# Kernel tuning notes

Hardware: AMD Instinct MI355X
Metric: run time of the kernel (lower is better)

Reference implementation:

```python
import jax, jax.numpy as jnp
import numpy as np
from jax import lax

ORDER = 2  # diffusion order per support, as in __init__(order=2)


def setup_inputs() -> dict:
    key = jax.random.key(0)
    k1, k2, k3 = jax.random.split(key, 3)
    N, C, V, L = 64, 32, 512, 13
    S, Kt, C_out = 3, 3, 32
    C_cat = (ORDER * S + 1) * C  # 224
    x = jax.random.normal(k1, (N, C, V, L), dtype=jnp.float32)
    support = jax.random.uniform(k2, (S, V, V), dtype=jnp.float32)
    # Conv2d(c_in=224, c_out=32, kernel=(1,Kt)) weights, PyTorch OIHW layout
    W = jax.random.normal(k3, (C_out, C_cat, 1, Kt), dtype=jnp.float32) * 0.02
    b = jnp.zeros((C_out,), dtype=jnp.float32)
    return {"x": x, "support": support, "W": W, "b": b}


def _nconv(x, A):
    # torch: A = A.T; einsum('ncvl,vw->ncwl', x, A.T)
    # => out[n,c,w,l] = sum_v A[w,v] * x[n,c,v,l]
    return jnp.einsum('ncvl,wv->ncwl', x, A)


def reference(x, support, W, b):
    out = [x]
    for s in range(support.shape[0]):  # small fixed support_len=3
        A = support[s]
        x1 = _nconv(x, A)
        out.append(x1)
        for _ in range(2, ORDER + 1):
            x1 = _nconv(x1, A)
            out.append(x1)
    h = jnp.concatenate(out, axis=1)  # [N, (order*S+1)*C, V, L]
    # Conv2d kernel (1, Kt), no padding, stride 1 -> temporal conv
    y = lax.conv_general_dilated(
        h, W, window_strides=(1, 1), padding='VALID',
        dimension_numbers=('NCHW', 'OIHW', 'NCHW'))
    y = y + b[None, :, None, None]
    # dropout is identity in eval mode
    return y
```

## Files before the change

kernel.cpp:

```cpp
#include <hip/hip_runtime.h>

typedef __attribute__((ext_vector_type(4))) float f32x4;
typedef __attribute__((ext_vector_type(8))) __bf16 bf16x8;
typedef __attribute__((ext_vector_type(4))) __bf16 bf16x4;
typedef __attribute__((ext_vector_type(4))) int i32x4;

#define SXE (26624 * 512)

__global__ __launch_bounds__(256)
void prep_x(const float* __restrict__ x, __bf16* __restrict__ Xv2,
            const float* __restrict__ A, __bf16* __restrict__ Ab) {
  const int vt = blockIdx.x, n = blockIdx.y, tid = threadIdx.x;
  if (vt < 12) {
    const int i = (n * 12 + vt) * 256 + tid;
    const float4 f = ((const float4*)A)[i];
    bf16x4 o;
    o[0] = (__bf16)f.x; o[1] = (__bf16)f.y; o[2] = (__bf16)f.z; o[3] = (__bf16)f.w;
    ((bf16x4*)Ab)[i] = o;
  }
  __shared__ float Xs[32 * 209];
  const float* src = x + ((size_t)n * 32) * 6656 + vt * 16 * 13;
  for (int i = tid; i < 32 * 208; i += 256) {
    const int c = i / 208, r = i - c * 208;
    Xs[c * 209 + r] = src[(size_t)c * 6656 + r];
  }
  __syncthreads();
  for (int j = tid; j < 416; j += 256) {
    const int c = j & 31, l = j >> 5;
    bf16x8 o8[2];
    #pragma unroll
    for (int v = 0; v < 16; ++v) o8[v >> 3][v & 7] = (__bf16)Xs[c * 209 + v * 13 + l];
    __bf16* d = Xv2 + (((size_t)n * 13 + l) * 32 + c) * 512 + vt * 16;
    *(bf16x8*)d = o8[0];
    *(bf16x8*)(d + 8) = o8[1];
  }
}

__global__ __launch_bounds__(512, 2)
void gemm_bf16(const __bf16* __restrict__ Ab, const __bf16* __restrict__ SRC,
               __bf16* __restrict__ DSTB, size_t srcStride, size_t dstStride, int cpx) {
  extern __shared__ char gsm[];
  const int tid = threadIdx.x;
  const int lane = tid & 63, wid = tid >> 6, q = lane >> 4, r16 = lane & 15;

  const int bid = blockIdx.x;
  const int lg = (bid & 7) * cpx + (bid >> 3);
  const int bx = lg / 6, r6 = lg % 6, s = r6 >> 1, by = r6 & 1;

  const __bf16* Amat = Ab + (size_t)s * 512 * 512;
  const __bf16* B = SRC + (size_t)s * srcStride;
  __bf16* D = DSTB + (size_t)s * dstStride;

  const int W0 = by * 256, B0 = bx * 256;
  const int wm = wid >> 2, wn = wid & 3;
  const int srow = lane >> 3, spos = lane & 7;

  f32x4 acc[8][4];
  #pragma unroll
  for (int m = 0; m < 8; ++m)
    #pragma unroll
    for (int n = 0; n < 4; ++n) acc[m][n] = {0.f, 0.f, 0.f, 0.f};

  auto STAGE = [&](int bufsel, int kt) {
    const int k0 = kt * 64;
    char* As = gsm + bufsel * 65536;
    char* Bs = As + 32768;
    #pragma unroll
    for (int i = 0; i < 4; ++i) {
      const int slot = i * 8 + wid;
      const int r = slot * 8 + srow;
      const int gc = spos ^ (r & 7);
      const __bf16* ga = Amat + (size_t)(W0 + r) * 512 + k0 + gc * 8;
      const __bf16* gb = B    + (size_t)(B0 + r) * 512 + k0 + gc * 8;
      __builtin_amdgcn_global_load_lds((const __attribute__((address_space(1))) unsigned int*)ga,
                                       (__attribute__((address_space(3))) unsigned int*)(As + slot * 1024 + lane * 16),
                                       16, 0, 0);
      __builtin_amdgcn_global_load_lds((const __attribute__((address_space(1))) unsigned int*)gb,
                                       (__attribute__((address_space(3))) unsigned int*)(Bs + slot * 1024 + lane * 16),
                                       16, 0, 0);
    }
  };

  STAGE(0, 0);
  __syncthreads();

  for (int t = 0; t < 8; ++t) {
    const int cur = t & 1;
    if (t < 7) STAGE(cur ^ 1, t + 1);
    const char* As = gsm + cur * 65536;
    const char* Bs = As + 32768;
    #pragma unroll
    for (int ks = 0; ks < 2; ++ks) {
      const int ch = ks * 4 + q;
      bf16x8 af[4], df[8];
      #pragma unroll
      for (int n = 0; n < 4; ++n) {
        const int r = wn * 64 + n * 16 + r16;
        af[n] = *(const bf16x8*)(As + r * 128 + ((ch ^ (r & 7)) << 4));
      }
      #pragma unroll
      for (int m = 0; m < 8; ++m) {
        const int r = wm * 128 + m * 16 + r16;
        df[m] = *(const bf16x8*)(Bs + r * 128 + ((ch ^ (r & 7)) << 4));
      }
      __builtin_amdgcn_s_setprio(1);
      #pragma unroll
      for (int m = 0; m < 8; ++m)
        #pragma unroll
        for (int n = 0; n < 4; ++n)
          acc[m][n] = __builtin_amdgcn_mfma_f32_16x16x32_bf16(af[n], df[m], acc[m][n], 0, 0, 0);
      __builtin_amdgcn_s_setprio(0);
    }
    __syncthreads();
  }

  #pragma unroll
  for (int m = 0; m < 8; ++m) {
    const int b = B0 + wm * 128 + m * 16 + r16;
    #pragma unroll
    for (int n = 0; n < 4; ++n) {
      const int w = W0 + wn * 64 + n * 16 + q * 4;
      bf16x4 o4;
      o4[0] = (__bf16)acc[m][n][0]; o4[1] = (__bf16)acc[m][n][1];
      o4[2] = (__bf16)acc[m][n][2]; o4[3] = (__bf16)acc[m][n][3];
      *(bf16x4*)(D + (size_t)b * 512 + w) = o4;
    }
  }
}

__global__ __launch_bounds__(256, 2)
void conv_kernel(const __bf16* __restrict__ Xv2, const __bf16* __restrict__ Y1,
                 const __bf16* __restrict__ Y2, const float* __restrict__ W,
                 const float* __restrict__ bias, float* __restrict__ y) {
  const int vt = blockIdx.x;
  const int n  = blockIdx.y;
  const int tid = threadIdx.x;
  const int lane = tid & 63, wave = tid >> 6, q = lane >> 4, r16 = lane & 15;

  __shared__ char sm[59392];
  char* Ws = sm + 53248;

  const __bf16* gsrc[7] = {Xv2, Y1, Y2, Y1 + (size_t)SXE, Y2 + (size_t)SXE,
                           Y1 + 2 * (size_t)SXE, Y2 + 2 * (size_t)SXE};

  f32x4 acc[11][2];
  #pragma unroll
  for (int t = 0; t < 11; ++t) { acc[t][0] = {0,0,0,0}; acc[t][1] = {0,0,0,0}; }

  const int vv = wave * 16 + r16;
  const int vch = vv >> 3;
  const int vlo = (vv & 7) * 2;
  const int cst = tid >> 3, hst = tid & 7;
  const size_t goff = ((size_t)cst << 9) + hst * 8;
  const int lds_off = cst * 128 + ((hst ^ ((cst >> 3) << 1)) << 4);
  const int gbase = q * 1024 + (((vch ^ (q << 1)) & 7) << 4) + vlo;

  const size_t base = ((size_t)n * 416) * 512 + vt * 64;

  i32x4 hreg[13];
  {
    const __bf16* src = gsrc[0] + base;
    #pragma unroll
    for (int l = 0; l < 13; ++l)
      hreg[l] = *(const i32x4*)(src + (size_t)l * 16384 + goff);
  }

  for (int g = 0; g < 7; ++g) {
    __syncthreads();
    #pragma unroll
    for (int l = 0; l < 13; ++l)
      *(i32x4*)(sm + l * 4096 + lds_off) = hreg[l];
    for (int idx = tid; idx < 768; idx += 256) {
      const int f = idx >> 7, rem2 = idx & 127, lw = rem2 >> 1, half = rem2 & 1;
      const int kt = f >> 1, of = f & 1;
      const int o = of * 16 + (lw & 15);
      const int cc = g * 32 + (lw >> 4) * 8 + half * 4;
      bf16x4 w4;
      #pragma unroll
      for (int j = 0; j < 4; ++j)
        w4[j] = (__bf16)W[((size_t)o * 224 + cc + j) * 3 + kt];
      *(bf16x4*)(Ws + idx * 8) = w4;
    }
    __syncthreads();

    if (g < 6) {
      const __bf16* srcn = gsrc[g + 1] + base;
      #pragma unroll
      for (int l = 0; l < 13; ++l)
        hreg[l] = *(const i32x4*)(srcn + (size_t)l * 16384 + goff);
    }

    bf16x8 a8[13];
    #pragma unroll
    for (int l = 0; l < 13; ++l) {
      bf16x8 a;
      #pragma unroll
      for (int j = 0; j < 8; ++j)
        a[j] = *(const __bf16*)(sm + l * 4096 + gbase + j * 128);
      a8[l] = a;
    }
    bf16x8 wf[6];
    #pragma unroll
    for (int f = 0; f < 6; ++f)
      wf[f] = *(const bf16x8*)(Ws + (f * 64 + lane) * 16);

    #pragma unroll
    for (int kt = 0; kt < 3; ++kt)
      #pragma unroll
      for (int of = 0; of < 2; ++of)
        #pragma unroll
        for (int t = 0; t < 11; ++t)
          acc[t][of] = __builtin_amdgcn_mfma_f32_16x16x32_bf16(a8[t + kt], wf[kt * 2 + of], acc[t][of], 0, 0, 0);
  }

  float* Ds = (float*)sm;
  const int o16 = lane & 15;
  #pragma unroll
  for (int p = 0; p < 2; ++p) {
    __syncthreads();
    #pragma unroll
    for (int t = 0; t < 11; ++t) {
      const int vbase = wave * 16 + q * 4;
      #pragma unroll
      for (int rg = 0; rg < 4; ++rg)
        Ds[o16 * 708 + (vbase + rg) * 11 + t] = acc[t][p][rg];
    }
    __syncthreads();
    #pragma unroll
    for (int i = 0; i < 11; ++i) {
      const int cg = tid + i * 256;
      const int oo = cg / 176, ch = cg - oo * 176;
      f32x4 v4 = *(const f32x4*)(Ds + oo * 708 + ch * 4);
      const float bo = bias[p * 16 + oo];
      v4[0] += bo; v4[1] += bo; v4[2] += bo; v4[3] += bo;
      float* yp = y + (((size_t)n * 32 + p * 16 + oo) * 512 + vt * 64) * 11 + ch * 4;
      *(f32x4*)yp = v4;
    }
  }
}

extern "C" void kernel_launch(void* const* d_in, const int* in_sizes, int n_in,
                              void* d_out, int out_size, void* d_ws, size_t ws_size,
                              hipStream_t stream) {
  (void)in_sizes; (void)n_in; (void)out_size; (void)ws_size;
  const float* x = (const float*)d_in[0];
  const float* A = (const float*)d_in[1];
  const float* W = (const float*)d_in[2];
  const float* b = (const float*)d_in[3];
  float* y = (float*)d_out;

  char* ws = (char*)d_ws;
  const size_t SXB = (size_t)SXE * 2;
  __bf16* Xv2 = (__bf16*)ws;
  __bf16* Y1  = (__bf16*)(ws + SXB);
  __bf16* Y2  = (__bf16*)(ws + 4 * SXB);
  __bf16* Ab  = (__bf16*)(ws + 7 * SXB);

  prep_x<<<dim3(32, 64), 256, 0, stream>>>(x, Xv2, A, Ab);
  gemm_bf16<<<dim3(624), 512, 131072, stream>>>(Ab, Xv2, Y1, 0, (size_t)SXE, 78);
  gemm_bf16<<<dim3(624), 512, 131072, stream>>>(Ab, Y1, Y2, (size_t)SXE, (size_t)SXE, 78);
  conv_kernel<<<dim3(8, 64), 256, 0, stream>>>(Xv2, Y1, Y2, W, b, y);
}
```

Measured before the change: 208.6 us.

## Precompute squared supports and compute both diffusion hops in one GEMM launch

Adds a transpose kernel and a small GEMM that form A² for each support in bf16. The two dependent diffusion GEMM launches become a single launch that multiplies X by both A and A², writing all six outputs. The aim is to remove the serial dependency between the hops and reduce launch and tail overhead. In exchange it adds two small launches, one of which uses only 12 blocks, and rounds A² to bf16, which changes numerics slightly. The transposed and squared matrices are kept temporarily in the output buffer.

Result: no change. 208.8 us (+0.1%).

```diff
diff --git a/kernel.cpp b/kernel.cpp
--- a/kernel.cpp
+++ b/kernel.cpp
@@ -6,6 +6,7 @@
 typedef __attribute__((ext_vector_type(4))) int i32x4;
 
 #define SXE (26624 * 512)
+#define AMS 262144
 
 __global__ __launch_bounds__(256)
 void prep_x(const float* __restrict__ x, __bf16* __restrict__ Xv2,
@@ -36,20 +37,35 @@
   }
 }
 
+__global__ __launch_bounds__(256)
+void transA(const float* __restrict__ A, __bf16* __restrict__ Abt) {
+  const int ut = blockIdx.x, vt = blockIdx.y, s = blockIdx.z, tid = threadIdx.x;
+  __shared__ float T[64][65];
+  const float* Asrc = A + (size_t)s * AMS;
+  #pragma unroll
+  for (int p = 0; p < 16; ++p) {
+    const int rv = p * 4 + (tid >> 6), cu = tid & 63;
+    T[rv][cu] = Asrc[(size_t)(vt * 64 + rv) * 512 + ut * 64 + cu];
+  }
+  __syncthreads();
+  #pragma unroll
+  for (int p = 0; p < 16; ++p) {
+    const int ru = p * 4 + (tid >> 6), cv = tid & 63;
+    Abt[(size_t)s * AMS + (size_t)(ut * 64 + ru) * 512 + vt * 64 + cv] = (__bf16)T[cv][ru];
+  }
+}
+
 __global__ __launch_bounds__(512, 2)
-void gemm_bf16(const __bf16* __restrict__ Ab, const __bf16* __restrict__ SRC,
-               __bf16* __restrict__ DSTB, size_t srcStride, size_t dstStride, int cpx) {
+void gemm_asq(const __bf16* __restrict__ Abt, const __bf16* __restrict__ Ab,
+              __bf16* __restrict__ Ab2) {
   extern __shared__ char gsm[];
   const int tid = threadIdx.x;
   const int lane = tid & 63, wid = tid >> 6, q = lane >> 4, r16 = lane & 15;
-
-  const int bid = blockIdx.x;
-  const int lg = (bid & 7) * cpx + (bid >> 3);
-  const int bx = lg / 6, r6 = lg % 6, s = r6 >> 1, by = r6 & 1;
-
-  const __bf16* Amat = Ab + (size_t)s * 512 * 512;
-  const __bf16* B = SRC + (size_t)s * srcStride;
-  __bf16* D = DSTB + (size_t)s * dstStride;
+  const int bx = blockIdx.x, by = blockIdx.y, s = blockIdx.z;
+
+  const __bf16* Amat = Abt + (size_t)s * AMS;
+  const __bf16* B = Ab + (size_t)s * AMS;
+  __bf16* D = Ab2 + (size_t)s * AMS;
 
   const int W0 = by * 256, B0 = bx * 256;
   const int wm = wid >> 2, wn = wid & 3;
@@ -83,6 +99,94 @@
 
   STAGE(0, 0);
   __syncthreads();
+  for (int t = 0; t < 8; ++t) {
+    const int cur = t & 1;
+    if (t < 7) STAGE(cur ^ 1, t + 1);
+    const char* As = gsm + cur * 65536;
+    const char* Bs = As + 32768;
+    #pragma unroll
+    for (int ks = 0; ks < 2; ++ks) {
+      const int ch = ks * 4 + q;
+      bf16x8 af[4], df[8];
+      #pragma unroll
+      for (int n = 0; n < 4; ++n) {
+        const int r = wn * 64 + n * 16 + r16;
+        af[n] = *(const bf16x8*)(As + r * 128 + ((ch ^ (r & 7)) << 4));
+      }
+      #pragma unroll
+      for (int m = 0; m < 8; ++m) {
+        const int r = wm * 128 + m * 16 + r16;
+        df[m] = *(const bf16x8*)(Bs + r * 128 + ((ch ^ (r & 7)) << 4));
+      }
+      #pragma unroll
+      for (int m = 0; m < 8; ++m)
+        #pragma unroll
+        for (int n = 0; n < 4; ++n)
+          acc[m][n] = __builtin_amdgcn_mfma_f32_16x16x32_bf16(af[n], df[m], acc[m][n], 0, 0, 0);
+    }
+    __syncthreads();
+  }
+  #pragma unroll
+  for (int m = 0; m < 8; ++m) {
+    const int b = B0 + wm * 128 + m * 16 + r16;
+    #pragma unroll
+    for (int n = 0; n < 4; ++n) {
+      const int w = W0 + wn * 64 + n * 16 + q * 4;
+      bf16x4 o4;
+      o4[0] = (__bf16)acc[m][n][0]; o4[1] = (__bf16)acc[m][n][1];
+      o4[2] = (__bf16)acc[m][n][2]; o4[3] = (__bf16)acc[m][n][3];
+      *(bf16x4*)(D + (size_t)b * 512 + w) = o4;
+    }
+  }
+}
+
+__global__ __launch_bounds__(512, 2)
+void gemm_bf16(const __bf16* __restrict__ Ab, const __bf16* __restrict__ Ab2,
+               const __bf16* __restrict__ SRC, __bf16* __restrict__ Yb, int cpx) {
+  extern __shared__ char gsm[];
+  const int tid = threadIdx.x;
+  const int lane = tid & 63, wid = tid >> 6, q = lane >> 4, r16 = lane & 15;
+
+  const int bid = blockIdx.x;
+  const int lg = (bid & 7) * cpx + (bid >> 3);
+  const int bx = lg / 12, r12 = lg % 12, z = r12 >> 1, by = r12 & 1;
+
+  const __bf16* Amat = (z < 3) ? (Ab + (size_t)z * AMS) : (Ab2 + (size_t)(z - 3) * AMS);
+  const __bf16* B = SRC;
+  __bf16* D = Yb + (size_t)z * SXE;
+
+  const int W0 = by * 256, B0 = bx * 256;
+  const int wm = wid >> 2, wn = wid & 3;
+  const int srow = lane >> 3, spos = lane & 7;
+
+  f32x4 acc[8][4];
+  #pragma unroll
+  for (int m = 0; m < 8; ++m)
+    #pragma unroll
+    for (int n = 0; n < 4; ++n) acc[m][n] = {0.f, 0.f, 0.f, 0.f};
+
+  auto STAGE = [&](int bufsel, int kt) {
+    const int k0 = kt * 64;
+    char* As = gsm + bufsel * 65536;
+    char* Bs = As + 32768;
+    #pragma unroll
+    for (int i = 0; i < 4; ++i) {
+      const int slot = i * 8 + wid;
+      const int r = slot * 8 + srow;
+      const int gc = spos ^ (r & 7);
+      const __bf16* ga = Amat + (size_t)(W0 + r) * 512 + k0 + gc * 8;
+      const __bf16* gb = B    + (size_t)(B0 + r) * 512 + k0 + gc * 8;
+      __builtin_amdgcn_global_load_lds((const __attribute__((address_space(1))) unsigned int*)ga,
+                                       (__attribute__((address_space(3))) unsigned int*)(As + slot * 1024 + lane * 16),
+                                       16, 0, 0);
+      __builtin_amdgcn_global_load_lds((const __attribute__((address_space(1))) unsigned int*)gb,
+                                       (__attribute__((address_space(3))) unsigned int*)(Bs + slot * 1024 + lane * 16),
+                                       16, 0, 0);
+    }
+  };
+
+  STAGE(0, 0);
+  __syncthreads();
 
   for (int t = 0; t < 8; ++t) {
     const int cur = t & 1;
@@ -255,9 +359,12 @@
   __bf16* Y1  = (__bf16*)(ws + SXB);
   __bf16* Y2  = (__bf16*)(ws + 4 * SXB);
   __bf16* Ab  = (__bf16*)(ws + 7 * SXB);
+  __bf16* Ab2 = (__bf16*)d_out;
+  __bf16* Abt = (__bf16*)((char*)d_out + (4 << 20));
 
   prep_x<<<dim3(32, 64), 256, 0, stream>>>(x, Xv2, A, Ab);
-  gemm_bf16<<<dim3(624), 512, 131072, stream>>>(Ab, Xv2, Y1, 0, (size_t)SXE, 78);
-  gemm_bf16<<<dim3(624), 512, 131072, stream>>>(Ab, Y1, Y2, (size_t)SXE, (size_t)SXE, 78);
+  transA<<<dim3(8, 8, 3), 256, 0, stream>>>(A, Abt);
+  gemm_asq<<<dim3(2, 2, 3), 512, 131072, stream>>>(Abt, Ab, Ab2);
+  gemm_bf16<<<dim3(1248), 512, 131072, stream>>>(Ab, Ab2, Xv2, Y1, 156);
   conv_kernel<<<dim3(8, 64), 256, 0, stream>>>(Xv2, Y1, Y2, W, b, y);
 }
```
